# Kernel optimization log

Hardware: AMD Instinct MI355X
Metric: run time of the kernel (lower is better)

The kernel has to match this reference:

```python
import jax, jax.numpy as jnp
import numpy as np

NUM_HEADS = 6
KERNEL = 5
EPS = 1e-6


def _neighbor_idx(L, k):
    # NATTEN neighborhood: window start clamped so every query has exactly k neighbors
    starts = jnp.clip(jnp.arange(L) - k // 2, 0, L - k)
    return starts[:, None] + jnp.arange(k)  # [L, k]


def ada_rmsnorm(x, scale, w1, b1, w2, b2):
    # x: [B,C,D,H,W]; RMS over spatial dims, gamma from channel means via small MLP
    rms = jnp.sqrt(jnp.mean(x * x, axis=(2, 3, 4), keepdims=True) + EPS)
    xn = x / rms
    stats = jnp.mean(x, axis=(2, 3, 4))                 # [B,C]
    h = jax.nn.relu(stats @ w1.T + b1)                  # [B,2C]
    gamma = jax.nn.sigmoid(h @ w2.T + b2)               # [B,C]
    return xn * (scale * gamma[:, :, None, None, None])


def reference(x, scale1, n1_w1, n1_b1, n1_w2, n1_b2,
              qkv_w, qkv_b, proj_w, proj_b,
              scale2, n2_w1, n2_b1, n2_w2, n2_b2,
              mlp_w1, mlp_b1, mlp_w2, mlp_b2):
    B, C, D, H, W = x.shape
    nh_, k_ = NUM_HEADS, KERNEL
    hd = C // nh_
    K3 = k_ ** 3

    # --- norm1 + neighborhood attention ---
    h = ada_rmsnorm(x, scale1, n1_w1, n1_b1, n1_w2, n1_b2)
    t = jnp.transpose(h, (0, 2, 3, 4, 1))               # [B,D,H,W,C]
    qkv = t @ qkv_w.T + qkv_b                           # [B,D,H,W,3C]
    q, k, v = jnp.split(qkv, 3, axis=-1)
    q = q.reshape(B, D, H, W, nh_, hd)
    k = k.reshape(B, D, H, W, nh_, hd)
    v = v.reshape(B, D, H, W, nh_, hd)

    iD = _neighbor_idx(D, k_)
    iH = _neighbor_idx(H, k_)
    iW = _neighbor_idx(W, k_)
    nd = iD[:, None, None, :, None, None]               # [D,1,1,k,1,1]
    nhh = iH[None, :, None, None, :, None]              # [1,H,1,1,k,1]
    nw = iW[None, None, :, None, None, :]               # [1,1,W,1,1,k]

    k_nb = k[:, nd, nhh, nw].reshape(B, D, H, W, K3, nh_, hd)
    v_nb = v[:, nd, nhh, nw].reshape(B, D, H, W, K3, nh_, hd)

    scale_qk = hd ** -0.5
    scores = jnp.einsum('bdhwnc,bdhwknc->bdhwnk', q, k_nb) * scale_qk  # [B,D,H,W,heads,K3]
    p = jax.nn.softmax(scores, axis=-1)
    o = jnp.einsum('bdhwnk,bdhwknc->bdhwnc', p, v_nb).reshape(B, D, H, W, C)
    o = o @ proj_w.T + proj_b                            # output projection
    x = x + jnp.transpose(o, (0, 4, 1, 2, 3))

    # --- norm2 + 1x1-conv MLP (GELU exact) ---
    h2 = ada_rmsnorm(x, scale2, n2_w1, n2_b1, n2_w2, n2_b2)
    m = jnp.einsum('oc,bcdhw->bodhw', mlp_w1, h2) + mlp_b1[None, :, None, None, None]
    m = jax.nn.gelu(m, approximate=False)
    m = jnp.einsum('oc,bcdhw->bodhw', mlp_w2, m) + mlp_b2[None, :, None, None, None]
    return x + m


def setup_inputs() -> dict:
    key = jax.random.key(0)
    ks = jax.random.split(key, 16)
    B, C, D, H, W = 1, 192, 16, 16, 16
    hid = 2 * C
    mlp_h = int(4.0 * C)
    s = 0.02
    inp = {
        'x': jax.random.normal(ks[0], (B, C, D, H, W), jnp.float32),
        'scale1': jnp.ones((1, C, 1, 1, 1), jnp.float32),
        'n1_w1': jax.random.normal(ks[1], (hid, C), jnp.float32) * s,
        'n1_b1': jnp.zeros((hid,), jnp.float32),
        'n1_w2': jax.random.normal(ks[2], (C, hid), jnp.float32) * s,
        'n1_b2': jnp.zeros((C,), jnp.float32),
        'qkv_w': jax.random.normal(ks[3], (3 * C, C), jnp.float32) * s,
        'qkv_b': jnp.zeros((3 * C,), jnp.float32),
        'proj_w': jax.random.normal(ks[4], (C, C), jnp.float32) * s,
        'proj_b': jnp.zeros((C,), jnp.float32),
        'scale2': jnp.ones((1, C, 1, 1, 1), jnp.float32),
        'n2_w1': jax.random.normal(ks[5], (hid, C), jnp.float32) * s,
        'n2_b1': jnp.zeros((hid,), jnp.float32),
        'n2_w2': jax.random.normal(ks[6], (C, hid), jnp.float32) * s,
        'n2_b2': jnp.zeros((C,), jnp.float32),
        'mlp_w1': jax.random.normal(ks[7], (mlp_h, C), jnp.float32) * s,
        'mlp_b1': jnp.zeros((mlp_h,), jnp.float32),
        'mlp_w2': jax.random.normal(ks[8], (C, mlp_h), jnp.float32) * s,
        'mlp_b2': jnp.zeros((C,), jnp.float32),
    }
    return inp
```

## Files before the change

kernel.cpp:

```cpp
#include <hip/hip_runtime.h>
#include <hip/hip_bf16.h>
#include <cmath>


#define NPOS 4096
#define C_CH 192

typedef __bf16 bf16x8 __attribute__((ext_vector_type(8)));
typedef __bf16 bf16x4 __attribute__((ext_vector_type(4)));
typedef float  f32x4  __attribute__((ext_vector_type(4)));

__global__ __launch_bounds__(256) void prep_kernel(
    const float* __restrict__ s0, const float* __restrict__ s1,
    const float* __restrict__ s2, const float* __restrict__ s3,
    __bf16* __restrict__ d0, __bf16* __restrict__ d1,
    __bf16* __restrict__ d2, __bf16* __restrict__ d3,
    const float* __restrict__ x, float* __restrict__ sums, float* __restrict__ sumsq)
{
    int b = blockIdx.x;
    if (b < 432) {
        const float* src; __bf16* dst; int base;
        if (b < 108)      { src = s0; dst = d0; base = b; }
        else if (b < 144) { src = s1; dst = d1; base = b - 108; }
        else if (b < 288) { src = s2; dst = d2; base = b - 144; }
        else              { src = s3; dst = d3; base = b - 288; }
        int i = (base * 256 + threadIdx.x) * 4;
        float4 v = *(const float4*)(src + i);
        bf16x4 o = { (__bf16)v.x, (__bf16)v.y, (__bf16)v.z, (__bf16)v.w };
        *(bf16x4*)(dst + i) = o;
        return;
    }
    int c = b - 432;
    const float4* xc = (const float4*)(x + (size_t)c * NPOS);
    float a = 0.f, a2 = 0.f;
    for (int i = threadIdx.x; i < NPOS / 4; i += 256) {
        float4 v = xc[i];
        a  += v.x + v.y + v.z + v.w;
        a2 += v.x * v.x + v.y * v.y + v.z * v.z + v.w * v.w;
    }
    #pragma unroll
    for (int off = 32; off > 0; off >>= 1) {
        a  += __shfl_down(a, off);
        a2 += __shfl_down(a2, off);
    }
    __shared__ float ls[4], ls2[4];
    int wid = threadIdx.x >> 6;
    if ((threadIdx.x & 63) == 0) { ls[wid] = a; ls2[wid] = a2; }
    __syncthreads();
    if (threadIdx.x == 0) {
        float t = 0.f, t2 = 0.f;
        #pragma unroll
        for (int w = 0; w < 4; w++) { t += ls[w]; t2 += ls2[w]; }
        sums[c] = t; sumsq[c] = t2;
    }
}

__global__ __launch_bounds__(256) void stats_kernel(
    const float* __restrict__ x, float* __restrict__ sums, float* __restrict__ sumsq)
{
    int c = blockIdx.x;
    const float4* xc = (const float4*)(x + (size_t)c * NPOS);
    float a = 0.f, a2 = 0.f;
    for (int i = threadIdx.x; i < NPOS / 4; i += 256) {
        float4 v = xc[i];
        a  += v.x + v.y + v.z + v.w;
        a2 += v.x * v.x + v.y * v.y + v.z * v.z + v.w * v.w;
    }
    #pragma unroll
    for (int off = 32; off > 0; off >>= 1) {
        a  += __shfl_down(a, off);
        a2 += __shfl_down(a2, off);
    }
    __shared__ float ls[4], ls2[4];
    int wid = threadIdx.x >> 6;
    if ((threadIdx.x & 63) == 0) { ls[wid] = a; ls2[wid] = a2; }
    __syncthreads();
    if (threadIdx.x == 0) {
        float t = 0.f, t2 = 0.f;
        #pragma unroll
        for (int w = 0; w < 4; w++) { t += ls[w]; t2 += ls2[w]; }
        sums[c] = t; sumsq[c] = t2;
    }
}

__global__ __launch_bounds__(256) void convx_kernel(
    const float* __restrict__ x,
    const float* __restrict__ sums, const float* __restrict__ sumsq,
    const float* __restrict__ scale,
    const float* __restrict__ w1, const float* __restrict__ b1,
    const float* __restrict__ w2, const float* __restrict__ b2,
    __bf16* __restrict__ xb)
{
    __shared__ float stats[C_CH];
    __shared__ float h[384];
    __shared__ float gsl[C_CH];
    __shared__ float lds[192 * 17];
    int t = threadIdx.x;

    if (t < C_CH) stats[t] = sums[t] * (1.0f / (float)NPOS);
    __syncthreads();
    for (int j = t; j < 384; j += 256) {
        float acc = b1[j];
        const float* wr = w1 + (size_t)j * C_CH;
        #pragma unroll 4
        for (int c = 0; c < C_CH; c += 4) {
            float4 w4 = *(const float4*)(wr + c);
            acc += w4.x * stats[c] + w4.y * stats[c + 1] + w4.z * stats[c + 2] + w4.w * stats[c + 3];
        }
        h[j] = fmaxf(acc, 0.0f);
    }
    __syncthreads();
    if (t < C_CH) {
        float acc = b2[t];
        const float* wr = w2 + (size_t)t * 384;
        #pragma unroll 4
        for (int j = 0; j < 384; j += 4) {
            float4 w4 = *(const float4*)(wr + j);
            acc += w4.x * h[j] + w4.y * h[j + 1] + w4.z * h[j + 2] + w4.w * h[j + 3];
        }
        float g = 1.0f / (1.0f + __expf(-acc));
        float rms = sqrtf(sumsq[t] * (1.0f / (float)NPOS) + 1e-6f);
        gsl[t] = scale[t] * g / rms;
    }
    __syncthreads();

    int p0 = blockIdx.x * 16;
    for (int idx = t; idx < 192 * 4; idx += 256) {
        int row = idx >> 2, p4 = idx & 3;
        float4 v = *(const float4*)(x + (size_t)row * NPOS + p0 + p4 * 4);
        float g = gsl[row];
        lds[row * 17 + p4 * 4 + 0] = v.x * g;
        lds[row * 17 + p4 * 4 + 1] = v.y * g;
        lds[row * 17 + p4 * 4 + 2] = v.z * g;
        lds[row * 17 + p4 * 4 + 3] = v.w * g;
    }
    __syncthreads();
    for (int idx = t; idx < 48 * 16; idx += 256) {
        int c4 = idx >> 4, p = idx & 15;
        bf16x4 o;
        #pragma unroll
        for (int j = 0; j < 4; j++) o[j] = (__bf16)lds[(c4 * 4 + j) * 17 + p];
        *(bf16x4*)(xb + (size_t)(p0 + p) * 192 + c4 * 4) = o;
    }
}

template <int K, int EPI>
__global__ __launch_bounds__(256) void gemm_lds(
    const __bf16* __restrict__ W, const float* __restrict__ bias,
    const __bf16* __restrict__ X, void* __restrict__ out,
    const float* __restrict__ resid, int M,
    float* __restrict__ out_kv)
{
    constexpr int KC  = 192;
    constexpr int LDA = 200;
    __shared__ __bf16 al[64 * LDA];
    __shared__ __bf16 bl[64 * LDA];
    int t    = threadIdx.x;
    int lane = t & 63;
    int wv   = t >> 6;
    int r16  = lane & 15;
    int quad = lane >> 4;
    int wvm  = wv >> 1;
    int wvn  = wv & 1;
    int mBase = blockIdx.y * 64;
    int nBase = blockIdx.x * 64;

    f32x4 acc[2][2];
    #pragma unroll
    for (int i = 0; i < 2; i++)
        #pragma unroll
        for (int j = 0; j < 2; j++)
            acc[i][j] = (f32x4){0.f, 0.f, 0.f, 0.f};

    for (int k0 = 0; k0 < K; k0 += KC) {
        #pragma unroll
        for (int it = 0; it < 6; it++) {
            int c = it * 256 + t;
            int row = c / 24, off = c - row * 24;
            bf16x8 va = *(const bf16x8*)(W + (size_t)(mBase + row) * K + k0 + off * 8);
            *(bf16x8*)(al + row * LDA + off * 8) = va;
            bf16x8 vb = *(const bf16x8*)(X + (size_t)(nBase + row) * K + k0 + off * 8);
            *(bf16x8*)(bl + row * LDA + off * 8) = vb;
        }
        __syncthreads();
        #pragma unroll
        for (int ks = 0; ks < KC / 32; ks++) {
            bf16x8 a0 = *(const bf16x8*)(al + (wvm * 32 + r16) * LDA + ks * 32 + quad * 8);
            bf16x8 a1 = *(const bf16x8*)(al + (wvm * 32 + 16 + r16) * LDA + ks * 32 + quad * 8);
            bf16x8 b0 = *(const bf16x8*)(bl + (wvn * 32 + r16) * LDA + ks * 32 + quad * 8);
            bf16x8 b1 = *(const bf16x8*)(bl + (wvn * 32 + 16 + r16) * LDA + ks * 32 + quad * 8);
            acc[0][0] = __builtin_amdgcn_mfma_f32_16x16x32_bf16(a0, b0, acc[0][0], 0, 0, 0);
            acc[0][1] = __builtin_amdgcn_mfma_f32_16x16x32_bf16(a0, b1, acc[0][1], 0, 0, 0);
            acc[1][0] = __builtin_amdgcn_mfma_f32_16x16x32_bf16(a1, b0, acc[1][0], 0, 0, 0);
            acc[1][1] = __builtin_amdgcn_mfma_f32_16x16x32_bf16(a1, b1, acc[1][1], 0, 0, 0);
        }
        __syncthreads();
    }

    #pragma unroll
    for (int rt = 0; rt < 2; rt++) {
        int m0 = mBase + wvm * 32 + rt * 16 + quad * 4;
        float b0 = bias[m0], b1 = bias[m0 + 1], b2 = bias[m0 + 2], b3 = bias[m0 + 3];
        #pragma unroll
        for (int ct = 0; ct < 2; ct++) {
            int n = nBase + wvn * 32 + ct * 16 + r16;
            f32x4 a4 = acc[rt][ct];
            float g0 = a4[0] + b0, g1 = a4[1] + b1, g2 = a4[2] + b2, g3 = a4[3] + b3;
            if (EPI == 0) {
                int sect = m0 / 192;
                int o0 = m0 - sect * 192;
                if (sect == 0) {
                    const float qs = 0.17677669529663687f;
                    *(float4*)((float*)out + (size_t)n * 192 + o0) =
                        make_float4(g0 * qs, g1 * qs, g2 * qs, g3 * qs);
                } else {
                    *(float4*)(out_kv + (size_t)n * 384 + (sect - 1) * 192 + o0) =
                        make_float4(g0, g1, g2, g3);
                }
            } else if (EPI == 2) {
                float* o = (float*)out;
                size_t i0 = (size_t)m0 * NPOS + n;
                o[i0]            = g0 + resid[i0];
                o[i0 + NPOS]     = g1 + resid[i0 + NPOS];
                o[i0 + 2 * NPOS] = g2 + resid[i0 + 2 * NPOS];
                o[i0 + 3 * NPOS] = g3 + resid[i0 + 3 * NPOS];
            } else {
                bf16x4 v;
                v[0] = (__bf16)(0.5f * g0 * (1.0f + erff(g0 * 0.7071067811865475f)));
                v[1] = (__bf16)(0.5f * g1 * (1.0f + erff(g1 * 0.7071067811865475f)));
                v[2] = (__bf16)(0.5f * g2 * (1.0f + erff(g2 * 0.7071067811865475f)));
                v[3] = (__bf16)(0.5f * g3 * (1.0f + erff(g3 * 0.7071067811865475f)));
                *(bf16x4*)((__bf16*)out + (size_t)n * M + m0) = v;
            }
        }
    }
}

__global__ __launch_bounds__(256) void attn_kernel(
    const float* __restrict__ q, const float* __restrict__ kv, __bf16* __restrict__ o)
{
    int t = threadIdx.x;
    int pairIdx = blockIdx.x * 8 + (t >> 5);
    int sg   = (t >> 3) & 3;
    int lane = t & 7;
    int pos = pairIdx / 6;
    int head = pairIdx - pos * 6;
    int wq = pos & 15;
    int hq = (pos >> 4) & 15;
    int dq = pos >> 8;
    int d0 = min(max(dq - 2, 0), 11);
    int h0 = min(max(hq - 2, 0), 11);
    int w0 = min(max(wq - 2, 0), 11);

    const float* kvb = kv + head * 32 + lane * 4;
    float4 q4 = *(const float4*)(q + (size_t)pos * 192 + head * 32 + lane * 4);

    float l = 0.0f;
    float4 acc = make_float4(0.f, 0.f, 0.f, 0.f);

    for (int dh = sg; dh < 25; dh += 4) {
        int di = dh / 5;
        int hi = dh - di * 5;
        int np0 = (d0 + di) * 256 + (h0 + hi) * 16 + w0;
        const float* p = kvb + (size_t)np0 * 384;
        #pragma unroll
        for (int wi = 0; wi < 5; wi++) {
            float4 k4 = *(const float4*)p;
            float4 v4 = *(const float4*)(p + 192);
            float s = q4.x * k4.x + q4.y * k4.y + q4.z * k4.z + q4.w * k4.w;
            s += __shfl_xor(s, 1);
            s += __shfl_xor(s, 2);
            s += __shfl_xor(s, 4);
            float pr = __expf(s);
            l += pr;
            acc.x += pr * v4.x;
            acc.y += pr * v4.y;
            acc.z += pr * v4.z;
            acc.w += pr * v4.w;
            p += 384;
        }
    }

    #pragma unroll
    for (int off = 8; off <= 16; off <<= 1) {
        l     += __shfl_xor(l, off);
        acc.x += __shfl_xor(acc.x, off);
        acc.y += __shfl_xor(acc.y, off);
        acc.z += __shfl_xor(acc.z, off);
        acc.w += __shfl_xor(acc.w, off);
    }

    if (sg == 0) {
        float rl = 1.0f / l;
        bf16x4 ov = { (__bf16)(acc.x * rl), (__bf16)(acc.y * rl),
                      (__bf16)(acc.z * rl), (__bf16)(acc.w * rl) };
        *(bf16x4*)(o + (size_t)pos * 192 + head * 32 + lane * 4) = ov;
    }
}

extern "C" void kernel_launch(void* const* d_in, const int* in_sizes, int n_in,
                              void* d_out, int out_size, void* d_ws, size_t ws_size,
                              hipStream_t stream)
{
    const float* x      = (const float*)d_in[0];
    const float* scale1 = (const float*)d_in[1];
    const float* n1_w1  = (const float*)d_in[2];
    const float* n1_b1  = (const float*)d_in[3];
    const float* n1_w2  = (const float*)d_in[4];
    const float* n1_b2  = (const float*)d_in[5];
    const float* qkv_w  = (const float*)d_in[6];
    const float* qkv_b  = (const float*)d_in[7];
    const float* proj_w = (const float*)d_in[8];
    const float* proj_b = (const float*)d_in[9];
    const float* scale2 = (const float*)d_in[10];
    const float* n2_w1  = (const float*)d_in[11];
    const float* n2_b1  = (const float*)d_in[12];
    const float* n2_w2  = (const float*)d_in[13];
    const float* n2_b2  = (const float*)d_in[14];
    const float* mlp_w1 = (const float*)d_in[15];
    const float* mlp_b1 = (const float*)d_in[16];
    const float* mlp_w2 = (const float*)d_in[17];
    const float* mlp_b2 = (const float*)d_in[18];

    float* ws = (float*)d_ws;
    float*  q_buf  = ws;
    float*  kv_buf = ws + 786432;
    __bf16* m_buf  = (__bf16*)ws;
    __bf16* xb     = (__bf16*)(ws + 2359296);
    __bf16* o_attn = (__bf16*)(ws + 2752512);
    __bf16* qkv_wb = (__bf16*)(ws + 3145728);
    __bf16* proj_wb = qkv_wb + 110592;
    __bf16* m1_wb   = proj_wb + 36864;
    __bf16* m2_wb   = m1_wb + 147456;
    float*  sums   = ws + 3366912;
    float*  sumsq  = sums + 192;

    float* x2 = (float*)d_out;

    prep_kernel<<<624, 256, 0, stream>>>(qkv_w, proj_w, mlp_w1, mlp_w2,
                                         qkv_wb, proj_wb, m1_wb, m2_wb,
                                         x, sums, sumsq);
    convx_kernel<<<256, 256, 0, stream>>>(x, sums, sumsq, scale1,
                                          n1_w1, n1_b1, n1_w2, n1_b2, xb);
    gemm_lds<192, 0><<<dim3(64, 9), 256, 0, stream>>>(qkv_wb, qkv_b, xb, (void*)q_buf,
                                                      nullptr, 576, kv_buf);
    attn_kernel<<<3072, 256, 0, stream>>>(q_buf, kv_buf, o_attn);
    gemm_lds<192, 2><<<dim3(64, 3), 256, 0, stream>>>(proj_wb, proj_b, o_attn, (void*)x2,
                                                      x, 192, nullptr);
    stats_kernel<<<192, 256, 0, stream>>>(x2, sums, sumsq);
    convx_kernel<<<256, 256, 0, stream>>>(x2, sums, sumsq, scale2,
                                          n2_w1, n2_b1, n2_w2, n2_b2, xb);
    gemm_lds<192, 3><<<dim3(64, 12), 256, 0, stream>>>(m1_wb, mlp_b1, xb, (void*)m_buf,
                                                       nullptr, 768, nullptr);
    gemm_lds<768, 2><<<dim3(64, 3), 256, 0, stream>>>(m2_wb, mlp_b2, m_buf, (void*)x2,
                                                      x2, 192, nullptr);
}
```

Before: 199.5 us.

## Tile neighborhood attention with shared-memory K/V halo per block and head

Each block now handles a 2x4x4 query tile for one head. It first loads the 6x8x8 K/V halo into LDS as bf16 and then computes attention from shared memory instead of re-reading fp32 K/V from global memory for every query. Each thread keeps the full 32-dim head accumulator and splits the 125 neighbors across 8 lanes, then reduces with shuffles. This cuts redundant global K/V traffic, at the cost of heavy register use (64+ floats per thread), a large LDS footprint that may limit occupancy, and bf16 rounding of K/V.

```diff
diff --git a/kernel.cpp b/kernel.cpp
--- a/kernel.cpp
+++ b/kernel.cpp
@@ -239,63 +239,109 @@
 __global__ __launch_bounds__(256) void attn_kernel(
     const float* __restrict__ q, const float* __restrict__ kv, __bf16* __restrict__ o)
 {
+    constexpr int SLOT = 68;
+    __shared__ __bf16 kvs[384 * SLOT];
+    int bid  = blockIdx.x;
+    int head = bid % 6;
+    int T    = bid / 6;
+    int td = (T >> 4) * 2;
+    int th = ((T >> 2) & 3) * 4;
+    int tw = (T & 3) * 4;
+    int hd0 = min(max(td - 2, 0), 11);
+    int hh0 = min(max(th - 2, 0), 11);
+    int hw0 = min(max(tw - 2, 0), 11);
     int t = threadIdx.x;
-    int pairIdx = blockIdx.x * 8 + (t >> 5);
-    int sg   = (t >> 3) & 3;
-    int lane = t & 7;
-    int pos = pairIdx / 6;
-    int head = pairIdx - pos * 6;
-    int wq = pos & 15;
-    int hq = (pos >> 4) & 15;
-    int dq = pos >> 8;
+
+    #pragma unroll
+    for (int i = 0; i < 12; i++) {
+        int cidx = i * 256 + t;
+        int slot = cidx >> 3;
+        int ch8  = cidx & 7;
+        int a = slot >> 6;
+        int b = (slot >> 3) & 7;
+        int c = slot & 7;
+        int gd = min(hd0 + a, 15);
+        int gh = min(hh0 + b, 15);
+        int gw = min(hw0 + c, 15);
+        int gpos = (gd << 8) + (gh << 4) + gw;
+        int off = (ch8 < 4) ? (head * 32 + ch8 * 8)
+                            : (192 + head * 32 + (ch8 - 4) * 8);
+        const float* src = kv + (size_t)gpos * 384 + off;
+        float4 v0 = *(const float4*)src;
+        float4 v1 = *(const float4*)(src + 4);
+        bf16x8 o8 = { (__bf16)v0.x, (__bf16)v0.y, (__bf16)v0.z, (__bf16)v0.w,
+                      (__bf16)v1.x, (__bf16)v1.y, (__bf16)v1.z, (__bf16)v1.w };
+        *(bf16x8*)(kvs + slot * SLOT + ch8 * 8) = o8;
+    }
+    __syncthreads();
+
+    int pr = t >> 3;
+    int ln = t & 7;
+    int ld = pr >> 4, lh = (pr >> 2) & 3, lw = pr & 3;
+    int dq = td + ld, hq = th + lh, wq = tw + lw;
+    int pos = (dq << 8) + (hq << 4) + wq;
     int d0 = min(max(dq - 2, 0), 11);
     int h0 = min(max(hq - 2, 0), 11);
     int w0 = min(max(wq - 2, 0), 11);
-
-    const float* kvb = kv + head * 32 + lane * 4;
-    float4 q4 = *(const float4*)(q + (size_t)pos * 192 + head * 32 + lane * 4);
+    int base = (d0 - hd0) * 64 + (h0 - hh0) * 8 + (w0 - hw0);
+
+    float qv[32];
+    {
+        const float4* qp = (const float4*)(q + (size_t)pos * 192 + head * 32);
+        #pragma unroll
+        for (int i = 0; i < 8; i++) {
+            float4 v = qp[i];
+            qv[i * 4 + 0] = v.x; qv[i * 4 + 1] = v.y;
+            qv[i * 4 + 2] = v.z; qv[i * 4 + 3] = v.w;
+        }
+    }
 
     float l = 0.0f;
-    float4 acc = make_float4(0.f, 0.f, 0.f, 0.f);
-
-    for (int dh = sg; dh < 25; dh += 4) {
-        int di = dh / 5;
-        int hi = dh - di * 5;
-        int np0 = (d0 + di) * 256 + (h0 + hi) * 16 + w0;
-        const float* p = kvb + (size_t)np0 * 384;
-        #pragma unroll
-        for (int wi = 0; wi < 5; wi++) {
-            float4 k4 = *(const float4*)p;
-            float4 v4 = *(const float4*)(p + 192);
-            float s = q4.x * k4.x + q4.y * k4.y + q4.z * k4.z + q4.w * k4.w;
-            s += __shfl_xor(s, 1);
-            s += __shfl_xor(s, 2);
-            s += __shfl_xor(s, 4);
-            float pr = __expf(s);
-            l += pr;
-            acc.x += pr * v4.x;
-            acc.y += pr * v4.y;
-            acc.z += pr * v4.z;
-            acc.w += pr * v4.w;
-            p += 384;
-        }
-    }
-
-    #pragma unroll
-    for (int off = 8; off <= 16; off <<= 1) {
-        l     += __shfl_xor(l, off);
-        acc.x += __shfl_xor(acc.x, off);
-        acc.y += __shfl_xor(acc.y, off);
-        acc.z += __shfl_xor(acc.z, off);
-        acc.w += __shfl_xor(acc.w, off);
-    }
-
-    if (sg == 0) {
-        float rl = 1.0f / l;
-        bf16x4 ov = { (__bf16)(acc.x * rl), (__bf16)(acc.y * rl),
-                      (__bf16)(acc.z * rl), (__bf16)(acc.w * rl) };
-        *(bf16x4*)(o + (size_t)pos * 192 + head * 32 + lane * 4) = ov;
-    }
+    float acc[32];
+    #pragma unroll
+    for (int i = 0; i < 32; i++) acc[i] = 0.0f;
+
+    #pragma unroll
+    for (int it = 0; it < 16; it++) {
+        int idx = ln + it * 8;
+        if (idx < 125) {
+            int di  = idx / 25;
+            int rem = idx - di * 25;
+            int hi  = rem / 5;
+            int wi  = rem - hi * 5;
+            const __bf16* kp = kvs + (base + di * 64 + hi * 8 + wi) * SLOT;
+            float s = 0.0f;
+            #pragma unroll
+            for (int j = 0; j < 4; j++) {
+                bf16x8 k8 = *(const bf16x8*)(kp + j * 8);
+                #pragma unroll
+                for (int e = 0; e < 8; e++)
+                    s += qv[j * 8 + e] * (float)k8[e];
+            }
+            float pw = __expf(s);
+            l += pw;
+            #pragma unroll
+            for (int j = 0; j < 4; j++) {
+                bf16x8 v8 = *(const bf16x8*)(kp + 32 + j * 8);
+                #pragma unroll
+                for (int e = 0; e < 8; e++)
+                    acc[j * 8 + e] += pw * (float)v8[e];
+            }
+        }
+    }
+
+    #pragma unroll
+    for (int off = 1; off <= 4; off <<= 1) {
+        l += __shfl_xor(l, off);
+        #pragma unroll
+        for (int ch = 0; ch < 32; ch++)
+            acc[ch] += __shfl_xor(acc[ch], off);
+    }
+
+    float rl = 1.0f / l;
+    bf16x4 ov = { (__bf16)(acc[ln * 4 + 0] * rl), (__bf16)(acc[ln * 4 + 1] * rl),
+                  (__bf16)(acc[ln * 4 + 2] * rl), (__bf16)(acc[ln * 4 + 3] * rl) };
+    *(bf16x4*)(o + (size_t)pos * 192 + head * 32 + ln * 4) = ov;
 }
 
 extern "C" void kernel_launch(void* const* d_in, const int* in_sizes, int n_in,
@@ -344,7 +390,7 @@
                                           n1_w1, n1_b1, n1_w2, n1_b2, xb);
     gemm_lds<192, 0><<<dim3(64, 9), 256, 0, stream>>>(qkv_wb, qkv_b, xb, (void*)q_buf,
                                                       nullptr, 576, kv_buf);
-    attn_kernel<<<3072, 256, 0, stream>>>(q_buf, kv_buf, o_attn);
+    attn_kernel<<<768, 256, 0, stream>>>(q_buf, kv_buf, o_attn);
     gemm_lds<192, 2><<<dim3(64, 3), 256, 0, stream>>>(proj_wb, proj_b, o_attn, (void*)x2,
                                                       x, 192, nullptr);
     stats_kernel<<<192, 256, 0, stream>>>(x2, sums, sumsq);
```

After: 226.3 us. +13.4%, slower.
